# Performance work log

Hardware: AMD Instinct MI355X
Metric: run time of the kernel (lower is better)

## Reference

```python
import jax, jax.numpy as jnp
import numpy as np

B, S, H = 2, 2048, 1024
E, K, F = 64, 8, 512
NORM_TOPK = True
CAP_FACTOR = 2.0


def setup_inputs() -> dict:
    key = jax.random.key(0)
    k0, k1, k2, k3, k4 = jax.random.split(key, 5)
    s_h = 1.0 / np.sqrt(H)
    s_f = 1.0 / np.sqrt(F)
    return {
        "hidden_states": jax.random.normal(k0, (B, S, H), jnp.float32),
        "w_gate": jax.random.normal(k1, (H, E), jnp.float32) * s_h,  # gate: Linear(H->E), no bias
        "w1": jax.random.normal(k2, (E, H, F), jnp.float32) * s_h,   # gate_proj per expert
        "w3": jax.random.normal(k3, (E, H, F), jnp.float32) * s_h,   # up_proj per expert
        "w2": jax.random.normal(k4, (E, F, H), jnp.float32) * s_f,   # down_proj per expert
    }


def reference(hidden_states, w_gate, w1, w3, w2):
    b, s, h = hidden_states.shape
    e = w_gate.shape[1]
    t = b * s
    x = hidden_states.reshape(t, h)
    router_logits = x @ w_gate                                   # [T, E]
    probs = jax.nn.softmax(router_logits.astype(jnp.float32), axis=-1)
    topw, sel = jax.lax.top_k(probs, K)                          # [T, K]
    if NORM_TOPK:
        topw = topw / jnp.sum(topw, axis=-1, keepdims=True)
    topw = topw.astype(x.dtype)

    a = t * K                                                    # total assignments
    c = int(CAP_FACTOR * a / e)                                  # static per-expert capacity
    sel_flat = sel.reshape(a)
    w_flat = topw.reshape(a)
    tok = jnp.repeat(jnp.arange(t), K)
    order = jnp.argsort(sel_flat, stable=True)                   # group assignments by expert
    e_s, t_s, w_s = sel_flat[order], tok[order], w_flat[order]
    counts = jnp.bincount(sel_flat, length=e)
    starts = jnp.cumsum(counts) - counts
    pos = jnp.arange(a) - starts[e_s]                            # position within expert group
    valid = pos < c
    slot = jnp.where(valid, e_s * c + pos, e * c)                # overflow -> dropped sentinel slot

    # dispatch: gather tokens into per-expert contiguous buffer [E, C, H]
    buf = jnp.zeros((e * c + 1, h), x.dtype).at[slot].set(x[t_s])
    xb = buf[: e * c].reshape(e, c, h)
    # grouped gated-SiLU MLP per expert
    g = jnp.einsum('ech,ehf->ecf', xb, w1)
    u = jnp.einsum('ech,ehf->ecf', xb, w3)
    yb = jnp.einsum('ecf,efh->ech', jax.nn.silu(g) * u, w2).reshape(e * c, h)
    # combine: weighted scatter-add back to tokens
    contrib = yb[jnp.minimum(slot, e * c - 1)] * (w_s * valid.astype(x.dtype))[:, None]
    out = jnp.zeros((t, h), x.dtype).at[t_s].add(contrib)
    return out.reshape(b, s, h), router_logits
```

## Files before the change

kernel.cpp:

```cpp
#include <hip/hip_runtime.h>
#include <hip/hip_bf16.h>

#define T_TOK 4096
#define H_DIM 1024
#define E_EXP 64
#define TOPK  8
#define F_DIM 512
#define CAP   1024
#define A_TOT (T_TOK * TOPK)

typedef _Float16 f16;
typedef _Float16 f16x2 __attribute__((ext_vector_type(2)));
typedef _Float16 f16x4 __attribute__((ext_vector_type(4)));
typedef _Float16 f16x8 __attribute__((ext_vector_type(8)));
typedef float    f32x4 __attribute__((ext_vector_type(4)));

__global__ __launch_bounds__(256) void pack_w_kernel(
    const float* __restrict__ src, f16* __restrict__ dst, int Kd, int Nd)
{
    __shared__ f16 tile[32][132];
    const int tid = threadIdx.x;
    const int nb = Nd >> 7;
    const int kb = Kd >> 5;
    const int b = blockIdx.x;
    const int n0  = (b % nb) * 128;
    const int kt0 = (b / nb) % kb;
    const int e   = b / (nb * kb);

    const float* s = src + ((size_t)e * Kd + kt0 * 32) * Nd + n0;
    #pragma unroll
    for (int rep = 0; rep < 4; ++rep) {
        int idx = rep * 256 + tid;
        int r = idx >> 5, c = (idx & 31) * 4;
        float4 v = *(const float4*)(s + (size_t)r * Nd + c);
        f16x4 h; h[0] = (f16)v.x; h[1] = (f16)v.y; h[2] = (f16)v.z; h[3] = (f16)v.w;
        *(f16x4*)&tile[r][c] = h;
    }
    __syncthreads();
    const int lane = tid & 63, wv = tid >> 6;
    #pragma unroll
    for (int ci = 0; ci < 2; ++ci) {
        int c = wv + ci * 4;
        f16x8 v;
        #pragma unroll
        for (int j = 0; j < 8; ++j)
            v[j] = tile[(lane >> 4) * 8 + j][c * 16 + (lane & 15)];
        int nt = (n0 >> 4) + c;
        size_t chunk = ((size_t)e * (Nd >> 4) + nt) * kb + kt0;
        *(f16x8*)(dst + chunk * 512 + lane * 8) = v;
    }
}

__global__ __launch_bounds__(256) void router_kernel(
    const float* __restrict__ x, const float* __restrict__ wg,
    float* __restrict__ logits_out, int* __restrict__ sel,
    float* __restrict__ wgtA, f16* __restrict__ xh)
{
    __shared__ float xs[16][128];
    __shared__ float ls[16][65];
    const int tid = threadIdx.x;
    const int e  = tid & 63;
    const int tg = tid >> 6;
    const int tb = blockIdx.x * 16;

    float acc[4] = {0.f, 0.f, 0.f, 0.f};
    for (int h0 = 0; h0 < H_DIM; h0 += 128) {
        {
            int r  = tid >> 4;
            int c0 = (tid & 15) * 8;
            const float4* src = (const float4*)(x + (size_t)(tb + r) * H_DIM + h0 + c0);
            float4 v0 = src[0], v1 = src[1];
            *(float4*)&xs[r][c0]     = v0;
            *(float4*)&xs[r][c0 + 4] = v1;
            f16x8 hv;
            hv[0] = (f16)v0.x; hv[1] = (f16)v0.y; hv[2] = (f16)v0.z; hv[3] = (f16)v0.w;
            hv[4] = (f16)v1.x; hv[5] = (f16)v1.y; hv[6] = (f16)v1.z; hv[7] = (f16)v1.w;
            *(f16x8*)(xh + (size_t)(tb + r) * H_DIM + h0 + c0) = hv;
        }
        __syncthreads();
        for (int hh = 0; hh < 128; ++hh) {
            float w = wg[(size_t)(h0 + hh) * E_EXP + e];
            #pragma unroll
            for (int i = 0; i < 4; ++i)
                acc[i] = fmaf(xs[tg * 4 + i][hh], w, acc[i]);
        }
        __syncthreads();
    }
    #pragma unroll
    for (int i = 0; i < 4; ++i) {
        int tt = tg * 4 + i;
        logits_out[(size_t)(tb + tt) * E_EXP + e] = acc[i];
        ls[tt][e] = acc[i];
    }
    __syncthreads();
    if (tid < 16) {
        int tt = tid;
        float lv[8]; int li[8];
        for (int k = 0; k < 8; ++k) {
            float m = -1e30f; int mi = 0;
            for (int j = 0; j < 64; ++j) {
                float v = ls[tt][j];
                if (v > m) { m = v; mi = j; }
            }
            lv[k] = m; li[k] = mi;
            ls[tt][mi] = -1e30f;
        }
        float s = 0.f, wv[8];
        for (int k = 0; k < 8; ++k) { wv[k] = __expf(lv[k] - lv[0]); s += wv[k]; }
        float inv = 1.f / s;
        for (int k = 0; k < 8; ++k) {
            int a = (tb + tt) * TOPK + k;
            sel[a]  = li[k];
            wgtA[a] = wv[k] * inv;
        }
    }
}

__global__ __launch_bounds__(256) void build_lists_kernel(
    const int* __restrict__ sel, const float* __restrict__ wgtA,
    int* __restrict__ tok_list, float* __restrict__ wgt_list,
    int* __restrict__ counts)
{
    __shared__ int sc[256];
    const int e = blockIdx.x;
    const int tid = threadIdx.x;
    const int per = A_TOT / 256;
    const int a0 = tid * per;
    int cnt = 0;
    for (int i = 0; i < per; ++i) cnt += (sel[a0 + i] == e) ? 1 : 0;
    sc[tid] = cnt;
    __syncthreads();
    for (int s = 1; s < 256; s <<= 1) {
        int v = (tid >= s) ? sc[tid - s] : 0;
        __syncthreads();
        sc[tid] += v;
        __syncthreads();
    }
    int total = sc[255];
    int pos = sc[tid] - cnt;
    if (tid == 0) counts[e] = (total < CAP) ? total : CAP;
    for (int i = 0; i < per; ++i) {
        int a = a0 + i;
        if (sel[a] == e) {
            if (pos < CAP) {
                tok_list[e * CAP + pos] = a >> 3;
                wgt_list[e * CAP + pos] = wgtA[a];
            }
            pos++;
        }
    }
}

#define MFMA16(a, b, c) __builtin_amdgcn_mfma_f32_16x16x32_f16(a, b, c, 0, 0, 0)

__global__ __launch_bounds__(256) void gemm1_kernel(
    const f16* __restrict__ xh, const f16* __restrict__ w1p,
    const f16* __restrict__ w3p, const int* __restrict__ tok_list,
    const int* __restrict__ counts, f16* __restrict__ P)
{
    const int id = blockIdx.x;
    const int x7 = id & 7, r = id >> 3;
    const int ft = r & 7, mt = (r >> 3) & 15, eh = r >> 7;
    const int e = x7 + 8 * eh;
    const int cnt = counts[e];
    const int m0 = mt * 64;
    if (m0 >= cnt) return;
    const int bf = ft * 64;

    __shared__ f16 Xs[2][64][72];
    __shared__ int tok_s[64];

    const int tid = threadIdx.x;
    const int lane = tid & 63, wv = tid >> 6;
    const int jj = lane & 15, qq = lane >> 4;
    const int sr = tid >> 3, sc = (tid & 7) * 8;

    if (tid < 64) {
        int m = m0 + tid;
        tok_s[tid] = (m < cnt) ? tok_list[e * CAP + m] : tok_list[e * CAP];
    }
    __syncthreads();
    const size_t rowA = (size_t)tok_s[sr] * H_DIM + sc;
    const size_t rowB = (size_t)tok_s[sr + 32] * H_DIM + sc;

    const f16* w1b = w1p + (((size_t)e * 32 + ft * 4 + wv) * 32) * 512 + lane * 8;
    const f16* w3b = w3p + (((size_t)e * 32 + ft * 4 + wv) * 32) * 512 + lane * 8;

    f32x4 accG[4], accU[4];
    #pragma unroll
    for (int i = 0; i < 4; ++i) {
        accG[i] = (f32x4){0.f, 0.f, 0.f, 0.f};
        accU[i] = (f32x4){0.f, 0.f, 0.f, 0.f};
    }

    {
        f16x8 a = *(const f16x8*)(xh + rowA);
        f16x8 b = *(const f16x8*)(xh + rowB);
        *(f16x8*)&Xs[0][sr][sc]      = a;
        *(f16x8*)&Xs[0][sr + 32][sc] = b;
    }
    f16x8 cG0 = *(const f16x8*)(w1b);
    f16x8 cG1 = *(const f16x8*)(w1b + 512);
    f16x8 cU0 = *(const f16x8*)(w3b);
    f16x8 cU1 = *(const f16x8*)(w3b + 512);

    #pragma unroll
    for (int it = 0; it < 16; ++it) {
        const int k0 = it * 64;
        __syncthreads();
        f16x8 xn0, xn1, nG0, nG1, nU0, nU1;
        if (it < 15) {
            xn0 = *(const f16x8*)(xh + rowA + k0 + 64);
            xn1 = *(const f16x8*)(xh + rowB + k0 + 64);
            size_t kg = (size_t)(2 * it + 2) * 512;
            nG0 = *(const f16x8*)(w1b + kg);
            nG1 = *(const f16x8*)(w1b + kg + 512);
            nU0 = *(const f16x8*)(w3b + kg);
            nU1 = *(const f16x8*)(w3b + kg + 512);
        }
        const int buf = it & 1;
        #pragma unroll
        for (int m2 = 0; m2 < 4; ++m2) {
            f16x8 a0 = *(const f16x8*)&Xs[buf][m2 * 16 + jj][qq * 8];
            f16x8 a1 = *(const f16x8*)&Xs[buf][m2 * 16 + jj][32 + qq * 8];
            accG[m2] = MFMA16(a0, cG0, accG[m2]);
            accU[m2] = MFMA16(a0, cU0, accU[m2]);
            accG[m2] = MFMA16(a1, cG1, accG[m2]);
            accU[m2] = MFMA16(a1, cU1, accU[m2]);
        }
        if (it < 15) {
            *(f16x8*)&Xs[buf ^ 1][sr][sc]      = xn0;
            *(f16x8*)&Xs[buf ^ 1][sr + 32][sc] = xn1;
            cG0 = nG0; cG1 = nG1; cU0 = nU0; cU1 = nU1;
        }
    }
    #pragma unroll
    for (int m2 = 0; m2 < 4; ++m2) {
        #pragma unroll
        for (int rr = 0; rr < 4; ++rr) {
            int row = m2 * 16 + qq * 4 + rr;
            float gg = accG[m2][rr], u = accU[m2][rr];
            float p = gg / (1.f + __expf(-gg)) * u;
            P[(size_t)(e * CAP + m0 + row) * F_DIM + bf + wv * 16 + jj] = (f16)p;
        }
    }
}

__global__ __launch_bounds__(256) void gemm2_kernel(
    const f16* __restrict__ P, const f16* __restrict__ w2p,
    const int* __restrict__ tok_list, const float* __restrict__ wgt_list,
    const int* __restrict__ counts, float* __restrict__ out)
{
    const int id = blockIdx.x;
    const int x7 = id & 7, r = id >> 3;
    const int ht = r & 7, mt = (r >> 3) & 15, eh = r >> 7;
    const int e = x7 + 8 * eh;
    const int cnt = counts[e];
    const int m0 = mt * 64;
    if (m0 >= cnt) return;
    const int h0 = ht * 128;

    __shared__ f16   Ps[2][64][72];
    __shared__ int   tok_s[64];
    __shared__ float wgt_s[64];

    const int tid = threadIdx.x;
    const int lane = tid & 63, wv = tid >> 6;
    const int jj = lane & 15, qq = lane >> 4;
    const int sr = tid >> 3, sc = (tid & 7) * 8;

    if (tid < 64) {
        int m = m0 + tid;
        tok_s[tid] = (m < cnt) ? tok_list[e * CAP + m] : 0;
        wgt_s[tid] = (m < cnt) ? wgt_list[e * CAP + m] : 0.f;
    }

    const size_t pbase = (size_t)(e * CAP + m0) * F_DIM;
    const f16* wA = w2p + (((size_t)e * 64 + ht * 8 + wv) * 16) * 512 + lane * 8;
    const f16* wB = w2p + (((size_t)e * 64 + ht * 8 + wv + 4) * 16) * 512 + lane * 8;

    f32x4 accA[4], accB[4];
    #pragma unroll
    for (int i = 0; i < 4; ++i) {
        accA[i] = (f32x4){0.f, 0.f, 0.f, 0.f};
        accB[i] = (f32x4){0.f, 0.f, 0.f, 0.f};
    }

    {
        f16x8 a = *(const f16x8*)(P + pbase + (size_t)sr * F_DIM + sc);
        f16x8 b = *(const f16x8*)(P + pbase + (size_t)(sr + 32) * F_DIM + sc);
        *(f16x8*)&Ps[0][sr][sc]      = a;
        *(f16x8*)&Ps[0][sr + 32][sc] = b;
    }
    f16x8 cA0 = *(const f16x8*)(wA);
    f16x8 cA1 = *(const f16x8*)(wA + 512);
    f16x8 cB0 = *(const f16x8*)(wB);
    f16x8 cB1 = *(const f16x8*)(wB + 512);

    #pragma unroll
    for (int it = 0; it < 8; ++it) {
        const int k0 = it * 64;
        __syncthreads();
        f16x8 pn0, pn1, nA0, nA1, nB0, nB1;
        if (it < 7) {
            pn0 = *(const f16x8*)(P + pbase + (size_t)sr * F_DIM + k0 + 64 + sc);
            pn1 = *(const f16x8*)(P + pbase + (size_t)(sr + 32) * F_DIM + k0 + 64 + sc);
            size_t kg = (size_t)(2 * it + 2) * 512;
            nA0 = *(const f16x8*)(wA + kg);
            nA1 = *(const f16x8*)(wA + kg + 512);
            nB0 = *(const f16x8*)(wB + kg);
            nB1 = *(const f16x8*)(wB + kg + 512);
        }
        const int buf = it & 1;
        #pragma unroll
        for (int m2 = 0; m2 < 4; ++m2) {
            f16x8 a0 = *(const f16x8*)&Ps[buf][m2 * 16 + jj][qq * 8];
            f16x8 a1 = *(const f16x8*)&Ps[buf][m2 * 16 + jj][32 + qq * 8];
            accA[m2] = MFMA16(a0, cA0, accA[m2]);
            accB[m2] = MFMA16(a0, cB0, accB[m2]);
            accA[m2] = MFMA16(a1, cA1, accA[m2]);
            accB[m2] = MFMA16(a1, cB1, accB[m2]);
        }
        if (it < 7) {
            *(f16x8*)&Ps[buf ^ 1][sr][sc]      = pn0;
            *(f16x8*)&Ps[buf ^ 1][sr + 32][sc] = pn1;
            cA0 = nA0; cA1 = nA1; cB0 = nB0; cB1 = nB1;
        }
    }
    #pragma unroll
    for (int m2 = 0; m2 < 4; ++m2) {
        #pragma unroll
        for (int rr = 0; rr < 4; ++rr) {
            int row = m2 * 16 + qq * 4 + rr;
            if (m0 + row < cnt) {
                float w = wgt_s[row];
                float* obase = &out[(size_t)tok_s[row] * H_DIM + h0 + wv * 16 + jj];
                unsafeAtomicAdd(obase,      accA[m2][rr] * w);
                unsafeAtomicAdd(obase + 64, accB[m2][rr] * w);
            }
        }
    }
}

extern "C" void kernel_launch(void* const* d_in, const int* in_sizes, int n_in,
                              void* d_out, int out_size, void* d_ws, size_t ws_size,
                              hipStream_t stream) {
    const float* x  = (const float*)d_in[0];
    const float* wg = (const float*)d_in[1];
    const float* w1 = (const float*)d_in[2];
    const float* w3 = (const float*)d_in[3];
    const float* w2 = (const float*)d_in[4];

    float* out    = (float*)d_out;
    float* logits = out + (size_t)T_TOK * H_DIM;

    char* ws = (char*)d_ws;
    int*   sel      = (int*)  (ws);
    float* wgtA     = (float*)(ws + (128 << 10));
    int*   tok_list = (int*)  (ws + (256 << 10));
    float* wgt_list = (float*)(ws + (512 << 10));
    int*   counts   = (int*)  (ws + (768 << 10));
    f16*   xh       = (f16*)  (ws + (size_t)(1 << 20));
    f16*   P        = (f16*)  (ws + (size_t)(9 << 20));
    f16*   w1p      = (f16*)  (ws + (size_t)(73 << 20));
    f16*   w3p      = (f16*)  (ws + (size_t)(137 << 20));
    f16*   w2p      = (f16*)  (ws + (size_t)(201 << 20));

    hipMemsetAsync(out, 0, (size_t)T_TOK * H_DIM * sizeof(float), stream);
    pack_w_kernel<<<8192, 256, 0, stream>>>(w1, w1p, H_DIM, F_DIM);
    pack_w_kernel<<<8192, 256, 0, stream>>>(w3, w3p, H_DIM, F_DIM);
    pack_w_kernel<<<8192, 256, 0, stream>>>(w2, w2p, F_DIM, H_DIM);
    router_kernel<<<T_TOK / 16, 256, 0, stream>>>(x, wg, logits, sel, wgtA, xh);
    build_lists_kernel<<<E_EXP, 256, 0, stream>>>(sel, wgtA, tok_list, wgt_list, counts);
    gemm1_kernel<<<8192, 256, 0, stream>>>(xh, w1p, w3p, tok_list, counts, P);
    gemm2_kernel<<<8192, 256, 0, stream>>>(P, w2p, tok_list, wgt_list, counts, out);
}
```

Baseline: 711.8 us.

## Replace atomic scatter-add with expert output buffer and gather combine kernel

gemm2 now writes unweighted per-expert outputs in f16 to a buffer Y. A new combine kernel gathers each token's up to eight expert rows through a per-assignment slot map and applies the routing weights. This removes the fp32 atomic scatter into the output and the output memset, at the cost of an extra f16 round trip through memory. Y reuses workspace space that held the packed w1/w3 weights, which are dead after gemm1. The weight pack kernel is also rewritten to skip shared memory: each lane does strided per-element loads of one 16x32 chunk. Those loads are less coalesced than the old float4 tile loads.

```diff
diff --git a/kernel.cpp b/kernel.cpp
--- a/kernel.cpp
+++ b/kernel.cpp
@@ -10,45 +10,27 @@
 #define A_TOT (T_TOK * TOPK)
 
 typedef _Float16 f16;
-typedef _Float16 f16x2 __attribute__((ext_vector_type(2)));
-typedef _Float16 f16x4 __attribute__((ext_vector_type(4)));
 typedef _Float16 f16x8 __attribute__((ext_vector_type(8)));
 typedef float    f32x4 __attribute__((ext_vector_type(4)));
 
 __global__ __launch_bounds__(256) void pack_w_kernel(
     const float* __restrict__ src, f16* __restrict__ dst, int Kd, int Nd)
 {
-    __shared__ f16 tile[32][132];
-    const int tid = threadIdx.x;
-    const int nb = Nd >> 7;
-    const int kb = Kd >> 5;
-    const int b = blockIdx.x;
-    const int n0  = (b % nb) * 128;
-    const int kt0 = (b / nb) % kb;
-    const int e   = b / (nb * kb);
-
-    const float* s = src + ((size_t)e * Kd + kt0 * 32) * Nd + n0;
-    #pragma unroll
-    for (int rep = 0; rep < 4; ++rep) {
-        int idx = rep * 256 + tid;
-        int r = idx >> 5, c = (idx & 31) * 4;
-        float4 v = *(const float4*)(s + (size_t)r * Nd + c);
-        f16x4 h; h[0] = (f16)v.x; h[1] = (f16)v.y; h[2] = (f16)v.z; h[3] = (f16)v.w;
-        *(f16x4*)&tile[r][c] = h;
-    }
-    __syncthreads();
+    const int tid  = threadIdx.x;
     const int lane = tid & 63, wv = tid >> 6;
-    #pragma unroll
-    for (int ci = 0; ci < 2; ++ci) {
-        int c = wv + ci * 4;
-        f16x8 v;
-        #pragma unroll
-        for (int j = 0; j < 8; ++j)
-            v[j] = tile[(lane >> 4) * 8 + j][c * 16 + (lane & 15)];
-        int nt = (n0 >> 4) + c;
-        size_t chunk = ((size_t)e * (Nd >> 4) + nt) * kb + kt0;
-        *(f16x8*)(dst + chunk * 512 + lane * 8) = v;
-    }
+    const int kbs = __builtin_ctz(Kd >> 5);
+    const int nts = __builtin_ctz(Nd >> 4);
+    const int chunk = blockIdx.x * 4 + wv;
+    const int kt = chunk & ((1 << kbs) - 1);
+    const int en = chunk >> kbs;
+    const int nt = en & ((1 << nts) - 1);
+    const int e  = en >> nts;
+    const int jj = lane & 15, qq = lane >> 4;
+    const float* s = src + ((size_t)e * Kd + kt * 32 + qq * 8) * Nd + nt * 16 + jj;
+    f16x8 v;
+    #pragma unroll
+    for (int j = 0; j < 8; ++j) v[j] = (f16)s[(size_t)j * Nd];
+    *(f16x8*)(dst + (size_t)chunk * 512 + lane * 8) = v;
 }
 
 __global__ __launch_bounds__(256) void router_kernel(
@@ -117,8 +99,8 @@
 }
 
 __global__ __launch_bounds__(256) void build_lists_kernel(
-    const int* __restrict__ sel, const float* __restrict__ wgtA,
-    int* __restrict__ tok_list, float* __restrict__ wgt_list,
+    const int* __restrict__ sel,
+    int* __restrict__ tok_list, int* __restrict__ slotA,
     int* __restrict__ counts)
 {
     __shared__ int sc[256];
@@ -144,7 +126,9 @@
         if (sel[a] == e) {
             if (pos < CAP) {
                 tok_list[e * CAP + pos] = a >> 3;
-                wgt_list[e * CAP + pos] = wgtA[a];
+                slotA[a] = e * CAP + pos;
+            } else {
+                slotA[a] = -1;
             }
             pos++;
         }
@@ -248,8 +232,7 @@
 
 __global__ __launch_bounds__(256) void gemm2_kernel(
     const f16* __restrict__ P, const f16* __restrict__ w2p,
-    const int* __restrict__ tok_list, const float* __restrict__ wgt_list,
-    const int* __restrict__ counts, float* __restrict__ out)
+    const int* __restrict__ counts, f16* __restrict__ Y)
 {
     const int id = blockIdx.x;
     const int x7 = id & 7, r = id >> 3;
@@ -260,20 +243,12 @@
     if (m0 >= cnt) return;
     const int h0 = ht * 128;
 
-    __shared__ f16   Ps[2][64][72];
-    __shared__ int   tok_s[64];
-    __shared__ float wgt_s[64];
+    __shared__ f16 Ps[2][64][72];
 
     const int tid = threadIdx.x;
     const int lane = tid & 63, wv = tid >> 6;
     const int jj = lane & 15, qq = lane >> 4;
     const int sr = tid >> 3, sc = (tid & 7) * 8;
-
-    if (tid < 64) {
-        int m = m0 + tid;
-        tok_s[tid] = (m < cnt) ? tok_list[e * CAP + m] : 0;
-        wgt_s[tid] = (m < cnt) ? wgt_list[e * CAP + m] : 0.f;
-    }
 
     const size_t pbase = (size_t)(e * CAP + m0) * F_DIM;
     const f16* wA = w2p + (((size_t)e * 64 + ht * 8 + wv) * 16) * 512 + lane * 8;
@@ -327,19 +302,41 @@
             cA0 = nA0; cA1 = nA1; cB0 = nB0; cB1 = nB1;
         }
     }
+    f16* yb = Y + (size_t)(e * CAP + m0) * H_DIM + h0 + wv * 16 + jj;
     #pragma unroll
     for (int m2 = 0; m2 < 4; ++m2) {
         #pragma unroll
         for (int rr = 0; rr < 4; ++rr) {
             int row = m2 * 16 + qq * 4 + rr;
-            if (m0 + row < cnt) {
-                float w = wgt_s[row];
-                float* obase = &out[(size_t)tok_s[row] * H_DIM + h0 + wv * 16 + jj];
-                unsafeAtomicAdd(obase,      accA[m2][rr] * w);
-                unsafeAtomicAdd(obase + 64, accB[m2][rr] * w);
-            }
-        }
-    }
+            yb[(size_t)row * H_DIM]      = (f16)accA[m2][rr];
+            yb[(size_t)row * H_DIM + 64] = (f16)accB[m2][rr];
+        }
+    }
+}
+
+__global__ __launch_bounds__(256) void combine_kernel(
+    const f16* __restrict__ Y, const int* __restrict__ slotA,
+    const float* __restrict__ wgtA, float* __restrict__ out)
+{
+    const int tid = threadIdx.x;
+    const int t  = blockIdx.x * 2 + (tid >> 7);
+    const int hc = (tid & 127) * 8;
+    float acc[8] = {0.f, 0.f, 0.f, 0.f, 0.f, 0.f, 0.f, 0.f};
+    const int base = t * TOPK;
+    #pragma unroll
+    for (int k = 0; k < 8; ++k) {
+        int s   = slotA[base + k];
+        float w = wgtA[base + k];
+        if (s >= 0) {
+            f16x8 y = *(const f16x8*)(Y + (size_t)s * H_DIM + hc);
+            #pragma unroll
+            for (int j = 0; j < 8; ++j) acc[j] += w * (float)y[j];
+        }
+    }
+    float4 o0 = {acc[0], acc[1], acc[2], acc[3]};
+    float4 o1 = {acc[4], acc[5], acc[6], acc[7]};
+    *(float4*)(out + (size_t)t * H_DIM + hc)     = o0;
+    *(float4*)(out + (size_t)t * H_DIM + hc + 4) = o1;
 }
 
 extern "C" void kernel_launch(void* const* d_in, const int* in_sizes, int n_in,
@@ -358,20 +355,21 @@
     int*   sel      = (int*)  (ws);
     float* wgtA     = (float*)(ws + (128 << 10));
     int*   tok_list = (int*)  (ws + (256 << 10));
-    float* wgt_list = (float*)(ws + (512 << 10));
+    int*   slotA    = (int*)  (ws + (512 << 10));
     int*   counts   = (int*)  (ws + (768 << 10));
     f16*   xh       = (f16*)  (ws + (size_t)(1 << 20));
     f16*   P        = (f16*)  (ws + (size_t)(9 << 20));
     f16*   w1p      = (f16*)  (ws + (size_t)(73 << 20));
     f16*   w3p      = (f16*)  (ws + (size_t)(137 << 20));
     f16*   w2p      = (f16*)  (ws + (size_t)(201 << 20));
-
-    hipMemsetAsync(out, 0, (size_t)T_TOK * H_DIM * sizeof(float), stream);
-    pack_w_kernel<<<8192, 256, 0, stream>>>(w1, w1p, H_DIM, F_DIM);
-    pack_w_kernel<<<8192, 256, 0, stream>>>(w3, w3p, H_DIM, F_DIM);
-    pack_w_kernel<<<8192, 256, 0, stream>>>(w2, w2p, F_DIM, H_DIM);
+    f16*   Y        = (f16*)  (ws + (size_t)(73 << 20));
+
+    pack_w_kernel<<<16384, 256, 0, stream>>>(w1, w1p, H_DIM, F_DIM);
+    pack_w_kernel<<<16384, 256, 0, stream>>>(w3, w3p, H_DIM, F_DIM);
+    pack_w_kernel<<<16384, 256, 0, stream>>>(w2, w2p, F_DIM, H_DIM);
     router_kernel<<<T_TOK / 16, 256, 0, stream>>>(x, wg, logits, sel, wgtA, xh);
-    build_lists_kernel<<<E_EXP, 256, 0, stream>>>(sel, wgtA, tok_list, wgt_list, counts);
+    build_lists_kernel<<<E_EXP, 256, 0, stream>>>(sel, tok_list, slotA, counts);
     gemm1_kernel<<<8192, 256, 0, stream>>>(xh, w1p, w3p, tok_list, counts, P);
-    gemm2_kernel<<<8192, 256, 0, stream>>>(P, w2p, tok_list, wgt_list, counts, out);
-}
+    gemm2_kernel<<<8192, 256, 0, stream>>>(P, w2p, counts, Y);
+    combine_kernel<<<T_TOK / 2, 256, 0, stream>>>(Y, slotA, wgtA, out);
+}
```

Measured after the change: 661.2 us. 7.1% less time.
